# Performance work log

Hardware: AMD Instinct MI355X
Metric: run time of the kernel (lower is better)

Reference implementation:

```python
import jax, jax.numpy as jnp
import numpy as np

B, S, HIDDEN = 2, 2048, 2048
NUM_HEADS, NUM_KV_HEADS, HEAD_DIM = 16, 4, 128
Q_SIZE = NUM_HEADS * HEAD_DIM          # 2048
KV_SIZE = NUM_KV_HEADS * HEAD_DIM      # 512
ROPE_THETA = 10000.0
NEG = -1e30


def setup_inputs() -> dict:
    key = jax.random.key(0)
    k1, k2, k3 = jax.random.split(key, 3)
    hidden_states = jax.random.normal(k1, (B, S, HIDDEN), jnp.float32)
    w_qkv = jax.random.normal(k2, (HIDDEN, Q_SIZE + 2 * KV_SIZE), jnp.float32) / np.sqrt(HIDDEN)
    w_o = jax.random.normal(k3, (Q_SIZE, HIDDEN), jnp.float32) / np.sqrt(Q_SIZE)
    positions = jnp.broadcast_to(jnp.arange(S, dtype=jnp.int32), (B, S))
    return {"positions": positions, "hidden_states": hidden_states,
            "w_qkv": w_qkv, "w_o": w_o}


def _rope(x, positions):
    # x: [B, S, H, D], neox-style rotate-half rope over full head_dim
    d = x.shape[-1]
    inv_freq = 1.0 / (ROPE_THETA ** (jnp.arange(0, d, 2, dtype=jnp.float32) / d))
    ang = positions[..., None].astype(jnp.float32) * inv_freq      # [B, S, D/2]
    cos = jnp.cos(ang)[:, :, None, :]
    sin = jnp.sin(ang)[:, :, None, :]
    x1, x2 = jnp.split(x, 2, axis=-1)
    return jnp.concatenate([x1 * cos - x2 * sin, x2 * cos + x1 * sin], axis=-1)


def reference(positions, hidden_states, w_qkv, w_o):
    qkv = jnp.einsum('bsh,ho->bso', hidden_states, w_qkv)
    q, k, v = jnp.split(qkv, [Q_SIZE, Q_SIZE + KV_SIZE], axis=-1)
    q = q.reshape(B, S, NUM_HEADS, HEAD_DIM)
    k = k.reshape(B, S, NUM_KV_HEADS, HEAD_DIM)
    v = v.reshape(B, S, NUM_KV_HEADS, HEAD_DIM)
    q = _rope(q, positions)
    k = _rope(k, positions)
    rep = NUM_HEADS // NUM_KV_HEADS
    k = jnp.repeat(k, rep, axis=2)   # GQA expand -> [B, S, NUM_HEADS, D]
    v = jnp.repeat(v, rep, axis=2)
    scale = HEAD_DIM ** -0.5
    scores = jnp.einsum('bqhd,bkhd->bhqk', q, k) * scale   # [B, H, S, S]
    causal = jnp.tril(jnp.ones((S, S), dtype=bool))
    scores = jnp.where(causal, scores, NEG)
    probs = jax.nn.softmax(scores, axis=-1)
    attn = jnp.einsum('bhqk,bkhd->bqhd', probs, v).reshape(B, S, Q_SIZE)
    return jnp.einsum('bsq,qh->bsh', attn, w_o)
```

## Files before the change

### kernel.cpp

```cpp
#include <hip/hip_runtime.h>
#include <hip/hip_bf16.h>
#include <stdint.h>

#define BDIM 2
#define SDIM 2048
#define HID 2048
#define NH 16
#define NKV 4
#define HD 128
#define QSZ 2048
#define KVSZ 512
#define QKVW 3072
#define TOK (BDIM*SDIM)

typedef __attribute__((ext_vector_type(8))) short bf16x8;
typedef __attribute__((ext_vector_type(4))) float f32x4;
typedef __attribute__((ext_vector_type(16))) float f32x16;

__device__ __forceinline__ short f2bf(float f) {
  return (short)__bfloat16_as_ushort(__float2bfloat16(f));
}

__device__ __forceinline__ float exp2_fast(float x) {
  float r;
  asm("v_exp_f32 %0, %1" : "=v"(r) : "v"(x));
  return r;
}

__device__ __forceinline__ void gload_lds16(const void* g, void* lds) {
  __builtin_amdgcn_global_load_lds(
      (const __attribute__((address_space(1))) void*)g,
      (__attribute__((address_space(3))) void*)lds, 16, 0, 0);
}

__global__ __launch_bounds__(256) void k_cvt_bf16(const float* __restrict__ in,
                                                  short* __restrict__ out, int n) {
  int i = (blockIdx.x * 256 + threadIdx.x) * 4;
  if (i >= n) return;
  float4 v = *(const float4*)(in + i);
  short4 o; o.x = f2bf(v.x); o.y = f2bf(v.y); o.z = f2bf(v.z); o.w = f2bf(v.w);
  *(short4*)(out + i) = o;
}

__global__ __launch_bounds__(256) void k_transpose_cvt(const float* __restrict__ in,
                                                       short* __restrict__ out,
                                                       int R, int C) {
  __shared__ short tile[64][65];
  int k0 = blockIdx.y * 64;
  int n0 = blockIdx.x * 64;
  int t = threadIdx.x;
#pragma unroll
  for (int i = 0; i < 16; ++i) {
    int idx = i * 256 + t;
    int kk = idx >> 6, nn = idx & 63;
    tile[kk][nn] = f2bf(in[(size_t)(k0 + kk) * C + n0 + nn]);
  }
  __syncthreads();
#pragma unroll
  for (int i = 0; i < 16; ++i) {
    int idx = i * 256 + t;
    int nn = idx >> 6, kk = idx & 63;
    out[(size_t)(n0 + nn) * R + k0 + kk] = tile[kk][nn];
  }
}

__global__ __launch_bounds__(256) void k_gemm_bf16(const short* __restrict__ A,
                                                   const short* __restrict__ Bt,
                                                   float* __restrict__ C,
                                                   int M, int N, int K) {
  __shared__ char lds[128 * 32 * 2 * 2];
  char* As = lds;
  char* Bs = lds + 8192;
  const int tid = threadIdx.x;
  const int w = tid >> 6, l = tid & 63;
  const int lq = l & 15, g = l >> 4;
  const int m0 = blockIdx.y * 128, n0 = blockIdx.x * 128;
  const int wm = (w >> 1) * 64, wn = (w & 1) * 64;
  f32x4 acc[4][4] = {};

  const int nk = K >> 5;
  for (int kt = 0; kt < nk; ++kt) {
    const int k0 = kt * 32;
#pragma unroll
    for (int i = 0; i < 2; ++i) {
      int ch = (w + 4 * i) * 64 + l;
      int r = ch >> 2, cc = ch & 3;
      int gc = cc ^ ((r >> 1) & 3);
      gload_lds16(A + (size_t)(m0 + r) * K + k0 + gc * 8, As + (w + 4 * i) * 1024);
      gload_lds16(Bt + (size_t)(n0 + r) * K + k0 + gc * 8, Bs + (w + 4 * i) * 1024);
    }
    __syncthreads();
    bf16x8 af[4], bfr[4];
#pragma unroll
    for (int mi = 0; mi < 4; ++mi) {
      int row = wm + mi * 16 + lq;
      af[mi] = *(const bf16x8*)(As + row * 64 + ((g ^ ((row >> 1) & 3)) * 16));
    }
#pragma unroll
    for (int ni = 0; ni < 4; ++ni) {
      int row = wn + ni * 16 + lq;
      bfr[ni] = *(const bf16x8*)(Bs + row * 64 + ((g ^ ((row >> 1) & 3)) * 16));
    }
#pragma unroll
    for (int mi = 0; mi < 4; ++mi)
#pragma unroll
      for (int ni = 0; ni < 4; ++ni)
        acc[mi][ni] = __builtin_amdgcn_mfma_f32_16x16x32_bf16(af[mi], bfr[ni],
                                                              acc[mi][ni], 0, 0, 0);
    __syncthreads();
  }
#pragma unroll
  for (int mi = 0; mi < 4; ++mi)
#pragma unroll
    for (int ni = 0; ni < 4; ++ni)
#pragma unroll
      for (int r = 0; r < 4; ++r) {
        int row = m0 + wm + mi * 16 + 4 * g + r;
        int col = n0 + wn + ni * 16 + lq;
        C[(size_t)row * N + col] = acc[mi][ni][r];
      }
}

__global__ __launch_bounds__(256) void k_rope(const float* __restrict__ qkv,
                                              const int* __restrict__ pos,
                                              short* __restrict__ Qh,
                                              short* __restrict__ Kh,
                                              short* __restrict__ VT, int S) {
  const int bs = blockIdx.x;
  const int b = bs / S, s = bs % S;
  const int t = threadIdx.x;
  const float p = (float)pos[bs];
  const size_t base = (size_t)bs * QKVW;
  const float scale = 0.12751743920f;
#pragma unroll
  for (int pass = 0; pass < 4; ++pass) {
    int idx = pass * 256 + t;
    int hh = idx >> 6, dd = idx & 63;
    float invf = expf(-(float)dd * (9.210340371976184f / 64.0f));
    float ang = p * invf, sn, cs;
    sincosf(ang, &sn, &cs);
    float x1 = qkv[base + hh * 128 + dd];
    float x2 = qkv[base + hh * 128 + dd + 64];
    size_t o = ((size_t)(b * NH + hh) * S + s) * HD + dd;
    Qh[o] = f2bf((x1 * cs - x2 * sn) * scale);
    Qh[o + 64] = f2bf((x2 * cs + x1 * sn) * scale);
  }
  {
    int hh = t >> 6, dd = t & 63;
    float invf = expf(-(float)dd * (9.210340371976184f / 64.0f));
    float ang = p * invf, sn, cs;
    sincosf(ang, &sn, &cs);
    float x1 = qkv[base + QSZ + hh * 128 + dd];
    float x2 = qkv[base + QSZ + hh * 128 + dd + 64];
    size_t o = ((size_t)(b * NKV + hh) * S + s) * HD + dd;
    Kh[o] = f2bf(x1 * cs - x2 * sn);
    Kh[o + 64] = f2bf(x2 * cs + x1 * sn);
  }
#pragma unroll
  for (int pass = 0; pass < 2; ++pass) {
    int idx = pass * 256 + t;
    int hh = idx >> 7, d = idx & 127;
    VT[((size_t)(b * NKV + hh) * HD + d) * S + s] = f2bf(qkv[base + QSZ + KVSZ + idx]);
  }
}

__global__ __launch_bounds__(256, 3) void k_attn(const short* __restrict__ Qh,
                                                 const short* __restrict__ Kh,
                                                 const short* __restrict__ VT,
                                                 short* __restrict__ attn, int S) {
  __shared__ char lds[2][16384];
  const int tid = threadIdx.x;
  const int w = tid >> 6, l = tid & 63;
  const int l31 = l & 31, hi = l >> 5;
  const int nqc = S / 128;
  const int bid = blockIdx.x;
  const int b = bid / (NH * nqc);
  const int rem = bid % (NH * nqc);
  const int h = rem / nqc;
  const int qc = nqc - 1 - (rem % nqc);
  const int q0 = qc * 128 + w * 32;
  const int kvh = h >> 2;
  const short* Qp = Qh + (size_t)(b * NH + h) * S * HD;
  const short* Kp = Kh + (size_t)(b * NKV + kvh) * S * HD;
  const short* Vp = VT + (size_t)(b * NKV + kvh) * HD * S;

  bf16x8 qf[8];
#pragma unroll
  for (int kc = 0; kc < 8; ++kc)
    qf[kc] = *(const bf16x8*)(Qp + (size_t)(q0 + l31) * HD + kc * 16 + hi * 8);

  f32x16 o[4] = {};
  float mrun = -1e30f, lrun = 0.f;
  const int qabs = q0 + l31;
  const int ntu = qc * 4 + 4;

#define STAGE(bufi, c0_)                                                          \
  {                                                                               \
    char* Kb = lds[bufi];                                                         \
    char* Vb = lds[bufi] + 8192;                                                  \
    _Pragma("unroll")                                                             \
    for (int i = 0; i < 2; ++i) {                                                 \
      int id = (i * 4 + w) * 64 + l;                                              \
      int kr = id >> 4, c16 = id & 15;                                            \
      gload_lds16(Kp + (size_t)((c0_) + kr) * HD + ((c16 ^ (kr & 7)) * 8),        \
                  Kb + (i * 4 + w) * 1024);                                       \
      int vr = id >> 2, c4 = id & 3;                                              \
      gload_lds16(Vp + (size_t)vr * S + (c0_) + ((c4 ^ (vr & 3)) * 8),            \
                  Vb + (i * 4 + w) * 1024);                                       \
    }                                                                             \
  }

  STAGE(0, 0);
  asm volatile("s_waitcnt vmcnt(0)" ::: "memory");
  __builtin_amdgcn_s_barrier();

  for (int c = 0; c < ntu; ++c) {
    const int c0 = c * 32;
    const int cur = c & 1;
    if (c + 1 < ntu) STAGE(cur ^ 1, c0 + 32);
    const char* Ks = lds[cur];
    const char* Vs = lds[cur] + 8192;

    f32x16 st = {};
    __builtin_amdgcn_s_setprio(1);
#pragma unroll
    for (int kc = 0; kc < 8; ++kc) {
      bf16x8 kf = *(const bf16x8*)(Ks + l31 * 256 + (((kc * 2 + hi) ^ (l31 & 7)) * 16));
      st = __builtin_amdgcn_mfma_f32_32x32x16_bf16(kf, qf[kc], st, 0, 0, 0);
    }
    __builtin_amdgcn_s_setprio(0);
    float tmax = -1e30f;
#pragma unroll
    for (int r = 0; r < 16; ++r) {
      int kv = c0 + (r & 3) + 8 * (r >> 2) + 4 * hi;
      float sv = (kv <= qabs) ? st[r] : -1e30f;
      st[r] = sv;
      tmax = fmaxf(tmax, sv);
    }
    tmax = fmaxf(tmax, __shfl_xor(tmax, 32));
    if (!__all(tmax - mrun <= 8.0f)) {
      float mnew = fmaxf(mrun, tmax);
      float fac = exp2_fast(mrun - mnew);
      lrun *= fac;
#pragma unroll
      for (int d0 = 0; d0 < 4; ++d0) o[d0] = o[d0] * fac;
      mrun = mnew;
    }
    float sum = 0.f;
#pragma unroll
    for (int r = 0; r < 16; ++r) {
      float e = exp2_fast(st[r] - mrun);
      st[r] = e;
      sum += e;
    }
    sum += __shfl_xor(sum, 32);
    lrun += sum;
    __builtin_amdgcn_s_setprio(1);
#pragma unroll
    for (int j = 0; j < 2; ++j) {
      uint32_t W0 = (uint32_t)(uint16_t)f2bf(st[8 * j + 0]) |
                    ((uint32_t)(uint16_t)f2bf(st[8 * j + 1]) << 16);
      uint32_t W1 = (uint32_t)(uint16_t)f2bf(st[8 * j + 2]) |
                    ((uint32_t)(uint16_t)f2bf(st[8 * j + 3]) << 16);
      uint32_t W2 = (uint32_t)(uint16_t)f2bf(st[8 * j + 4]) |
                    ((uint32_t)(uint16_t)f2bf(st[8 * j + 5]) << 16);
      uint32_t W3 = (uint32_t)(uint16_t)f2bf(st[8 * j + 6]) |
                    ((uint32_t)(uint16_t)f2bf(st[8 * j + 7]) << 16);
      uint32_t Y0 = __shfl_xor(hi ? W0 : W2, 32);
      uint32_t Y1 = __shfl_xor(hi ? W1 : W3, 32);
      union { uint32_t u[4]; bf16x8 v; } pu;
      pu.u[0] = hi ? Y0 : W0;
      pu.u[1] = hi ? Y1 : W1;
      pu.u[2] = hi ? W2 : Y0;
      pu.u[3] = hi ? W3 : Y1;
#pragma unroll
      for (int d0 = 0; d0 < 4; ++d0) {
        int vr = d0 * 32 + l31;
        bf16x8 vf = *(const bf16x8*)(Vs + vr * 64 + (((j * 2 + hi) ^ (vr & 3)) * 16));
        o[d0] = __builtin_amdgcn_mfma_f32_32x32x16_bf16(vf, pu.v, o[d0], 0, 0, 0);
      }
    }
    __builtin_amdgcn_s_setprio(0);
    asm volatile("s_waitcnt vmcnt(0)" ::: "memory");
    __builtin_amdgcn_s_barrier();
  }
#undef STAGE
  float inv = 1.0f / lrun;
  size_t rowb = (size_t)(b * S + q0 + l31) * QSZ + h * HD;
#pragma unroll
  for (int d0 = 0; d0 < 4; ++d0)
#pragma unroll
    for (int gq = 0; gq < 4; ++gq) {
      short4 ov;
      ov.x = f2bf(o[d0][4 * gq + 0] * inv);
      ov.y = f2bf(o[d0][4 * gq + 1] * inv);
      ov.z = f2bf(o[d0][4 * gq + 2] * inv);
      ov.w = f2bf(o[d0][4 * gq + 3] * inv);
      *(short4*)(attn + rowb + d0 * 32 + 8 * gq + 4 * hi) = ov;
    }
}

extern "C" void kernel_launch(void* const* d_in, const int* in_sizes, int n_in,
                              void* d_out, int out_size, void* d_ws, size_t ws_size,
                              hipStream_t stream) {
  const int* positions = (const int*)d_in[0];
  const float* hidden = (const float*)d_in[1];
  const float* w_qkv = (const float*)d_in[2];
  const float* w_o = (const float*)d_in[3];
  float* out = (float*)d_out;

  char* ws = (char*)d_ws;
  short* X     = (short*)(ws);
  short* WqkvT = (short*)(ws + 16777216);
  short* WoT   = (short*)(ws + 29360128);
  float* QKV   = (float*)(ws + 37748736);
  short* Qh    = (short*)(ws + 88080384);
  short* Kh    = (short*)(ws + 104857600);
  short* VT    = (short*)(ws + 109051904);
  short* ATT   = (short*)(ws + 113246208);

  k_cvt_bf16<<<8192, 256, 0, stream>>>(hidden, X, TOK * HID);
  k_transpose_cvt<<<dim3(QKVW / 64, HID / 64), 256, 0, stream>>>(w_qkv, WqkvT, HID, QKVW);
  k_transpose_cvt<<<dim3(HID / 64, QSZ / 64), 256, 0, stream>>>(w_o, WoT, QSZ, HID);
  k_gemm_bf16<<<dim3(QKVW / 128, TOK / 128), 256, 0, stream>>>(X, WqkvT, QKV, TOK, QKVW, HID);
  k_rope<<<TOK, 256, 0, stream>>>(QKV, positions, Qh, Kh, VT, SDIM);
  k_attn<<<BDIM * NH * (SDIM / 128), 256, 0, stream>>>(Qh, Kh, VT, ATT, SDIM);
  k_gemm_bf16<<<dim3(HID / 128, TOK / 128), 256, 0, stream>>>(ATT, WoT, out, TOK, HID, QSZ);
}
```

Before: 270.7 us.

## Software-pipeline attention: overlap next tile's QK^T with current softmax and PV

Restructures the attention KV loop into a two-stage software pipeline. The QK^T MFMAs for tile c run alongside the softmax and PV of tile c-1, using two score registers that alternate. LDS goes to a triple buffer and prefetch moves two tiles ahead, which lowers the launch-bounds occupancy target from 3 to 2 blocks. The V-tile LDS swizzle also changes to (vr>>1)&3 to cut bank conflicts. The goal is to hide softmax latency behind matrix work, at the cost of more registers and LDS and fewer resident blocks.

```diff
diff --git a/kernel.cpp b/kernel.cpp
--- a/kernel.cpp
+++ b/kernel.cpp
@@ -164,11 +164,11 @@
   }
 }
 
-__global__ __launch_bounds__(256, 3) void k_attn(const short* __restrict__ Qh,
+__global__ __launch_bounds__(256, 2) void k_attn(const short* __restrict__ Qh,
                                                  const short* __restrict__ Kh,
                                                  const short* __restrict__ VT,
                                                  short* __restrict__ attn, int S) {
-  __shared__ char lds[2][16384];
+  __shared__ char lds[3][16384];
   const int tid = threadIdx.x;
   const int w = tid >> 6, l = tid & 63;
   const int l31 = l & 31, hi = l >> 5;
@@ -205,86 +205,110 @@
       gload_lds16(Kp + (size_t)((c0_) + kr) * HD + ((c16 ^ (kr & 7)) * 8),        \
                   Kb + (i * 4 + w) * 1024);                                       \
       int vr = id >> 2, c4 = id & 3;                                              \
-      gload_lds16(Vp + (size_t)vr * S + (c0_) + ((c4 ^ (vr & 3)) * 8),            \
+      gload_lds16(Vp + (size_t)vr * S + (c0_) + ((c4 ^ ((vr >> 1) & 3)) * 8),     \
                   Vb + (i * 4 + w) * 1024);                                       \
     }                                                                             \
   }
 
+#define QKT(ST, cc)                                                               \
+  {                                                                               \
+    const char* Ks = lds[(cc) % 3];                                               \
+    f32x16 _z = {};                                                               \
+    ST = _z;                                                                      \
+    __builtin_amdgcn_s_setprio(1);                                                \
+    _Pragma("unroll")                                                             \
+    for (int kc = 0; kc < 8; ++kc) {                                              \
+      bf16x8 kf = *(const bf16x8*)(Ks + l31 * 256 + (((kc * 2 + hi) ^ (l31 & 7)) * 16)); \
+      ST = __builtin_amdgcn_mfma_f32_32x32x16_bf16(kf, qf[kc], ST, 0, 0, 0);      \
+    }                                                                             \
+    __builtin_amdgcn_s_setprio(0);                                                \
+  }
+
+#define SMPV(ST, pc)                                                              \
+  {                                                                               \
+    const int c0p = (pc) * 32;                                                    \
+    const char* Vs = lds[(pc) % 3] + 8192;                                        \
+    float tmax = -1e30f;                                                          \
+    _Pragma("unroll")                                                             \
+    for (int r = 0; r < 16; ++r) {                                                \
+      int kv = c0p + (r & 3) + 8 * (r >> 2) + 4 * hi;                             \
+      float sv = (kv <= qabs) ? ST[r] : -1e30f;                                   \
+      ST[r] = sv;                                                                 \
+      tmax = fmaxf(tmax, sv);                                                     \
+    }                                                                             \
+    tmax = fmaxf(tmax, __shfl_xor(tmax, 32));                                     \
+    if (!__all(tmax - mrun <= 8.0f)) {                                            \
+      float mnew = fmaxf(mrun, tmax);                                             \
+      float fac = exp2_fast(mrun - mnew);                                         \
+      lrun *= fac;                                                                \
+      _Pragma("unroll")                                                           \
+      for (int d0 = 0; d0 < 4; ++d0) o[d0] = o[d0] * fac;                         \
+      mrun = mnew;                                                                \
+    }                                                                             \
+    float sum = 0.f;                                                              \
+    _Pragma("unroll")                                                             \
+    for (int r = 0; r < 16; ++r) {                                                \
+      float e = exp2_fast(ST[r] - mrun);                                          \
+      ST[r] = e;                                                                  \
+      sum += e;                                                                   \
+    }                                                                             \
+    sum += __shfl_xor(sum, 32);                                                   \
+    lrun += sum;                                                                  \
+    __builtin_amdgcn_s_setprio(1);                                                \
+    _Pragma("unroll")                                                             \
+    for (int j = 0; j < 2; ++j) {                                                 \
+      uint32_t W0 = (uint32_t)(uint16_t)f2bf(ST[8 * j + 0]) |                     \
+                    ((uint32_t)(uint16_t)f2bf(ST[8 * j + 1]) << 16);              \
+      uint32_t W1 = (uint32_t)(uint16_t)f2bf(ST[8 * j + 2]) |                     \
+                    ((uint32_t)(uint16_t)f2bf(ST[8 * j + 3]) << 16);              \
+      uint32_t W2 = (uint32_t)(uint16_t)f2bf(ST[8 * j + 4]) |                     \
+                    ((uint32_t)(uint16_t)f2bf(ST[8 * j + 5]) << 16);              \
+      uint32_t W3 = (uint32_t)(uint16_t)f2bf(ST[8 * j + 6]) |                     \
+                    ((uint32_t)(uint16_t)f2bf(ST[8 * j + 7]) << 16);              \
+      uint32_t Y0 = __shfl_xor(hi ? W0 : W2, 32);                                 \
+      uint32_t Y1 = __shfl_xor(hi ? W1 : W3, 32);                                 \
+      union { uint32_t u[4]; bf16x8 v; } pu;                                      \
+      pu.u[0] = hi ? Y0 : W0;                                                     \
+      pu.u[1] = hi ? Y1 : W1;                                                     \
+      pu.u[2] = hi ? W2 : Y0;                                                     \
+      pu.u[3] = hi ? W3 : Y1;                                                     \
+      _Pragma("unroll")                                                           \
+      for (int d0 = 0; d0 < 4; ++d0) {                                            \
+        int vr = d0 * 32 + l31;                                                   \
+        bf16x8 vf = *(const bf16x8*)(Vs + vr * 64 + (((j * 2 + hi) ^ ((vr >> 1) & 3)) * 16)); \
+        o[d0] = __builtin_amdgcn_mfma_f32_32x32x16_bf16(vf, pu.v, o[d0], 0, 0, 0); \
+      }                                                                           \
+    }                                                                             \
+    __builtin_amdgcn_s_setprio(0);                                                \
+  }
+
   STAGE(0, 0);
+  STAGE(1, 32);
   asm volatile("s_waitcnt vmcnt(0)" ::: "memory");
   __builtin_amdgcn_s_barrier();
-
-  for (int c = 0; c < ntu; ++c) {
-    const int c0 = c * 32;
-    const int cur = c & 1;
-    if (c + 1 < ntu) STAGE(cur ^ 1, c0 + 32);
-    const char* Ks = lds[cur];
-    const char* Vs = lds[cur] + 8192;
-
-    f32x16 st = {};
-    __builtin_amdgcn_s_setprio(1);
-#pragma unroll
-    for (int kc = 0; kc < 8; ++kc) {
-      bf16x8 kf = *(const bf16x8*)(Ks + l31 * 256 + (((kc * 2 + hi) ^ (l31 & 7)) * 16));
-      st = __builtin_amdgcn_mfma_f32_32x32x16_bf16(kf, qf[kc], st, 0, 0, 0);
-    }
-    __builtin_amdgcn_s_setprio(0);
-    float tmax = -1e30f;
-#pragma unroll
-    for (int r = 0; r < 16; ++r) {
-      int kv = c0 + (r & 3) + 8 * (r >> 2) + 4 * hi;
-      float sv = (kv <= qabs) ? st[r] : -1e30f;
-      st[r] = sv;
-      tmax = fmaxf(tmax, sv);
-    }
-    tmax = fmaxf(tmax, __shfl_xor(tmax, 32));
-    if (!__all(tmax - mrun <= 8.0f)) {
-      float mnew = fmaxf(mrun, tmax);
-      float fac = exp2_fast(mrun - mnew);
-      lrun *= fac;
-#pragma unroll
-      for (int d0 = 0; d0 < 4; ++d0) o[d0] = o[d0] * fac;
-      mrun = mnew;
-    }
-    float sum = 0.f;
-#pragma unroll
-    for (int r = 0; r < 16; ++r) {
-      float e = exp2_fast(st[r] - mrun);
-      st[r] = e;
-      sum += e;
-    }
-    sum += __shfl_xor(sum, 32);
-    lrun += sum;
-    __builtin_amdgcn_s_setprio(1);
-#pragma unroll
-    for (int j = 0; j < 2; ++j) {
-      uint32_t W0 = (uint32_t)(uint16_t)f2bf(st[8 * j + 0]) |
-                    ((uint32_t)(uint16_t)f2bf(st[8 * j + 1]) << 16);
-      uint32_t W1 = (uint32_t)(uint16_t)f2bf(st[8 * j + 2]) |
-                    ((uint32_t)(uint16_t)f2bf(st[8 * j + 3]) << 16);
-      uint32_t W2 = (uint32_t)(uint16_t)f2bf(st[8 * j + 4]) |
-                    ((uint32_t)(uint16_t)f2bf(st[8 * j + 5]) << 16);
-      uint32_t W3 = (uint32_t)(uint16_t)f2bf(st[8 * j + 6]) |
-                    ((uint32_t)(uint16_t)f2bf(st[8 * j + 7]) << 16);
-      uint32_t Y0 = __shfl_xor(hi ? W0 : W2, 32);
-      uint32_t Y1 = __shfl_xor(hi ? W1 : W3, 32);
-      union { uint32_t u[4]; bf16x8 v; } pu;
-      pu.u[0] = hi ? Y0 : W0;
-      pu.u[1] = hi ? Y1 : W1;
-      pu.u[2] = hi ? W2 : Y0;
-      pu.u[3] = hi ? W3 : Y1;
-#pragma unroll
-      for (int d0 = 0; d0 < 4; ++d0) {
-        int vr = d0 * 32 + l31;
-        bf16x8 vf = *(const bf16x8*)(Vs + vr * 64 + (((j * 2 + hi) ^ (vr & 3)) * 16));
-        o[d0] = __builtin_amdgcn_mfma_f32_32x32x16_bf16(vf, pu.v, o[d0], 0, 0, 0);
-      }
-    }
-    __builtin_amdgcn_s_setprio(0);
+  f32x16 stA, stB;
+  QKT(stA, 0);
+  STAGE(2, 64);
+
+  int c = 1;
+  while (true) {
+    QKT(stB, c);
+    SMPV(stA, c - 1);
     asm volatile("s_waitcnt vmcnt(0)" ::: "memory");
     __builtin_amdgcn_s_barrier();
-  }
+    if (c + 2 < ntu) STAGE((c + 2) % 3, (c + 2) * 32);
+    if (++c >= ntu) break;
+    QKT(stA, c);
+    SMPV(stB, c - 1);
+    asm volatile("s_waitcnt vmcnt(0)" ::: "memory");
+    __builtin_amdgcn_s_barrier();
+    if (c + 2 < ntu) STAGE((c + 2) % 3, (c + 2) * 32);
+    ++c;
+  }
+  SMPV(stB, ntu - 1);
 #undef STAGE
+#undef QKT
+#undef SMPV
   float inv = 1.0f / lrun;
   size_t rowb = (size_t)(b * S + q0 + l31) * QSZ + h * HD;
 #pragma unroll
```

New measurement: 279.4 us. 1.03x slower.

## Fuse RoPE, scaling and V transpose into the QKV GEMM epilogue

Applied to the files above, without the earlier changes.

Replaces the fp32 QKV GEMM plus separate RoPE kernel with one GEMM whose epilogue applies rotary embedding and Q scaling. It writes bf16 Q/K in head-major layout and V transposed directly, using a 128-wide N tile that matches one head so the two rotate-half partners sit in the same thread. This removes the fp32 QKV intermediate round trip through memory and one kernel launch. It also changes the LDS XOR swizzle for V tiles in the attention kernel to reduce bank conflicts. The new GEMM tiling (each warp 32 rows by 128 columns) may change register pressure and efficiency compared with the generic GEMM.

```diff
diff --git a/kernel.cpp b/kernel.cpp
--- a/kernel.cpp
+++ b/kernel.cpp
@@ -121,46 +121,97 @@
       }
 }
 
-__global__ __launch_bounds__(256) void k_rope(const float* __restrict__ qkv,
-                                              const int* __restrict__ pos,
-                                              short* __restrict__ Qh,
-                                              short* __restrict__ Kh,
-                                              short* __restrict__ VT, int S) {
-  const int bs = blockIdx.x;
-  const int b = bs / S, s = bs % S;
-  const int t = threadIdx.x;
-  const float p = (float)pos[bs];
-  const size_t base = (size_t)bs * QKVW;
-  const float scale = 0.12751743920f;
-#pragma unroll
-  for (int pass = 0; pass < 4; ++pass) {
-    int idx = pass * 256 + t;
-    int hh = idx >> 6, dd = idx & 63;
-    float invf = expf(-(float)dd * (9.210340371976184f / 64.0f));
-    float ang = p * invf, sn, cs;
-    sincosf(ang, &sn, &cs);
-    float x1 = qkv[base + hh * 128 + dd];
-    float x2 = qkv[base + hh * 128 + dd + 64];
-    size_t o = ((size_t)(b * NH + hh) * S + s) * HD + dd;
-    Qh[o] = f2bf((x1 * cs - x2 * sn) * scale);
-    Qh[o + 64] = f2bf((x2 * cs + x1 * sn) * scale);
-  }
-  {
-    int hh = t >> 6, dd = t & 63;
-    float invf = expf(-(float)dd * (9.210340371976184f / 64.0f));
-    float ang = p * invf, sn, cs;
-    sincosf(ang, &sn, &cs);
-    float x1 = qkv[base + QSZ + hh * 128 + dd];
-    float x2 = qkv[base + QSZ + hh * 128 + dd + 64];
-    size_t o = ((size_t)(b * NKV + hh) * S + s) * HD + dd;
-    Kh[o] = f2bf(x1 * cs - x2 * sn);
-    Kh[o + 64] = f2bf(x2 * cs + x1 * sn);
-  }
-#pragma unroll
-  for (int pass = 0; pass < 2; ++pass) {
-    int idx = pass * 256 + t;
-    int hh = idx >> 7, d = idx & 127;
-    VT[((size_t)(b * NKV + hh) * HD + d) * S + s] = f2bf(qkv[base + QSZ + KVSZ + idx]);
+__global__ __launch_bounds__(256) void k_gemm_qkv_rope(const short* __restrict__ A,
+                                                       const short* __restrict__ Bt,
+                                                       const int* __restrict__ pos,
+                                                       short* __restrict__ Qh,
+                                                       short* __restrict__ Kh,
+                                                       short* __restrict__ VT) {
+  __shared__ char lds[128 * 32 * 2 * 2];
+  char* As = lds;
+  char* Bs = lds + 8192;
+  const int tid = threadIdx.x;
+  const int w = tid >> 6, l = tid & 63;
+  const int lq = l & 15, g = l >> 4;
+  const int m0 = blockIdx.y * 128, n0 = blockIdx.x * 128;
+  const int K = HID, N = QKVW;
+  f32x4 acc[2][8] = {};
+
+  const int nk = K >> 5;
+  for (int kt = 0; kt < nk; ++kt) {
+    const int k0 = kt * 32;
+#pragma unroll
+    for (int i = 0; i < 2; ++i) {
+      int ch = (w + 4 * i) * 64 + l;
+      int r = ch >> 2, cc = ch & 3;
+      int gc = cc ^ ((r >> 1) & 3);
+      gload_lds16(A + (size_t)(m0 + r) * K + k0 + gc * 8, As + (w + 4 * i) * 1024);
+      gload_lds16(Bt + (size_t)(n0 + r) * K + k0 + gc * 8, Bs + (w + 4 * i) * 1024);
+    }
+    __syncthreads();
+    bf16x8 af[2], bfr[8];
+#pragma unroll
+    for (int mi = 0; mi < 2; ++mi) {
+      int row = w * 32 + mi * 16 + lq;
+      af[mi] = *(const bf16x8*)(As + row * 64 + ((g ^ ((row >> 1) & 3)) * 16));
+    }
+#pragma unroll
+    for (int ni = 0; ni < 8; ++ni) {
+      int row = ni * 16 + lq;
+      bfr[ni] = *(const bf16x8*)(Bs + row * 64 + ((g ^ ((row >> 1) & 3)) * 16));
+    }
+#pragma unroll
+    for (int mi = 0; mi < 2; ++mi)
+#pragma unroll
+      for (int ni = 0; ni < 8; ++ni)
+        acc[mi][ni] = __builtin_amdgcn_mfma_f32_16x16x32_bf16(af[mi], bfr[ni],
+                                                              acc[mi][ni], 0, 0, 0);
+    __syncthreads();
+  }
+
+  const int hx = blockIdx.x;
+  const int b = m0 >> 11;
+  if (hx < 20) {
+    const float qscale = 0.12751743920f;
+    const float sc = (hx < 16) ? qscale : 1.0f;
+    short* dst = (hx < 16) ? (Qh + (size_t)(b * NH + hx) * SDIM * HD)
+                           : (Kh + (size_t)(b * NKV + (hx - 16)) * SDIM * HD);
+    float invf[4];
+#pragma unroll
+    for (int ni = 0; ni < 4; ++ni)
+      invf[ni] = expf(-(float)(ni * 16 + lq) * (9.210340371976184f / 64.0f));
+#pragma unroll
+    for (int mi = 0; mi < 2; ++mi)
+#pragma unroll
+      for (int r = 0; r < 4; ++r) {
+        int row = m0 + w * 32 + mi * 16 + 4 * g + r;
+        int s = row & (SDIM - 1);
+        float p = (float)pos[row];
+        size_t hb = (size_t)s * HD;
+#pragma unroll
+        for (int ni = 0; ni < 4; ++ni) {
+          float sn, cs;
+          sincosf(p * invf[ni], &sn, &cs);
+          float x1 = acc[mi][ni][r], x2 = acc[mi][ni + 4][r];
+          dst[hb + ni * 16 + lq] = f2bf((x1 * cs - x2 * sn) * sc);
+          dst[hb + ni * 16 + lq + 64] = f2bf((x2 * cs + x1 * sn) * sc);
+        }
+      }
+  } else {
+    const int hv = hx - 20;
+    const int s00 = (m0 & (SDIM - 1)) + w * 32;
+#pragma unroll
+    for (int mi = 0; mi < 2; ++mi)
+#pragma unroll
+      for (int ni = 0; ni < 8; ++ni) {
+        int d = ni * 16 + lq;
+        int s0 = s00 + mi * 16 + 4 * g;
+        size_t vb = ((size_t)(b * NKV + hv) * HD + d) * SDIM + s0;
+        short4 ov;
+        ov.x = f2bf(acc[mi][ni][0]); ov.y = f2bf(acc[mi][ni][1]);
+        ov.z = f2bf(acc[mi][ni][2]); ov.w = f2bf(acc[mi][ni][3]);
+        *(short4*)(VT + vb) = ov;
+      }
   }
 }
 
@@ -205,7 +256,7 @@
       gload_lds16(Kp + (size_t)((c0_) + kr) * HD + ((c16 ^ (kr & 7)) * 8),        \
                   Kb + (i * 4 + w) * 1024);                                       \
       int vr = id >> 2, c4 = id & 3;                                              \
-      gload_lds16(Vp + (size_t)vr * S + (c0_) + ((c4 ^ (vr & 3)) * 8),            \
+      gload_lds16(Vp + (size_t)vr * S + (c0_) + ((c4 ^ ((vr >> 1) & 3)) * 8),     \
                   Vb + (i * 4 + w) * 1024);                                       \
     }                                                                             \
   }
@@ -276,7 +327,7 @@
 #pragma unroll
       for (int d0 = 0; d0 < 4; ++d0) {
         int vr = d0 * 32 + l31;
-        bf16x8 vf = *(const bf16x8*)(Vs + vr * 64 + (((j * 2 + hi) ^ (vr & 3)) * 16));
+        bf16x8 vf = *(const bf16x8*)(Vs + vr * 64 + (((j * 2 + hi) ^ ((vr >> 1) & 3)) * 16));
         o[d0] = __builtin_amdgcn_mfma_f32_32x32x16_bf16(vf, pu.v, o[d0], 0, 0, 0);
       }
     }
@@ -313,7 +364,6 @@
   short* X     = (short*)(ws);
   short* WqkvT = (short*)(ws + 16777216);
   short* WoT   = (short*)(ws + 29360128);
-  float* QKV   = (float*)(ws + 37748736);
   short* Qh    = (short*)(ws + 88080384);
   short* Kh    = (short*)(ws + 104857600);
   short* VT    = (short*)(ws + 109051904);
@@ -322,8 +372,8 @@
   k_cvt_bf16<<<8192, 256, 0, stream>>>(hidden, X, TOK * HID);
   k_transpose_cvt<<<dim3(QKVW / 64, HID / 64), 256, 0, stream>>>(w_qkv, WqkvT, HID, QKVW);
   k_transpose_cvt<<<dim3(HID / 64, QSZ / 64), 256, 0, stream>>>(w_o, WoT, QSZ, HID);
-  k_gemm_bf16<<<dim3(QKVW / 128, TOK / 128), 256, 0, stream>>>(X, WqkvT, QKV, TOK, QKVW, HID);
-  k_rope<<<TOK, 256, 0, stream>>>(QKV, positions, Qh, Kh, VT, SDIM);
+  k_gemm_qkv_rope<<<dim3(QKVW / 128, TOK / 128), 256, 0, stream>>>(X, WqkvT, positions,
+                                                                   Qh, Kh, VT);
   k_attn<<<BDIM * NH * (SDIM / 128), 256, 0, stream>>>(Qh, Kh, VT, ATT, SDIM);
   k_gemm_bf16<<<dim3(HID / 128, TOK / 128), 256, 0, stream>>>(ATT, WoT, out, TOK, HID, QSZ);
 }
```

After: 238.6 us. 1.13x faster.
